# Optimization experiments

Hardware: AMD Instinct MI355X
Metric: run time of the kernel (lower is better)

Reference implementation:

```python
import jax, jax.numpy as jnp
from jax import lax
import numpy as np

B, C, HH, WW = 8, 64, 128, 128
N = HH * WW
EPS = 1e-5


def _roll_h(xn, sign):
    # per-channel cyclic roll along H: out[b,c,h,w] = xn[b,c,(h - sign*c) % H, w]
    _, Cx, Hx, _ = xn.shape
    c = jnp.arange(Cx)[:, None]
    idx = (jnp.arange(Hx)[None, :] - sign * jnp.arange(Cx)[:, None]) % Hx  # (C,H)
    return xn[:, c, idx, :]


def _roll_w(xn, sign):
    return _roll_h(xn.transpose(0, 1, 3, 2), sign).transpose(0, 1, 3, 2)


def _ch_linear(xn, w, b):
    # nn.Linear over the channel dim of a BCHW tensor (token-MLP on (B,N,C))
    return jnp.einsum('bchw,cd->bdhw', xn, w) + b[None, :, None, None]


def _bn(xn, g, b):
    # BatchNorm2d, training-mode stats (biased var over B,H,W)
    m = xn.mean(axis=(0, 2, 3), keepdims=True)
    v = xn.var(axis=(0, 2, 3), keepdims=True)
    return (xn - m) * lax.rsqrt(v + EPS) * g[None, :, None, None] + b[None, :, None, None]


def _dwconv(xn, w, dil, pad):
    return lax.conv_general_dilated(xn, w, (1, 1), ((pad, pad), (pad, pad)),
                                    rhs_dilation=(dil, dil),
                                    dimension_numbers=('NCHW', 'OIHW', 'NCHW'),
                                    feature_group_count=xn.shape[1])


def _pc(xn, w):
    # 1x1 pointwise conv, no bias; w: (C_out, C_in)
    return jnp.einsum('bchw,oc->bohw', xn, w)


def lgff_forward(x, fc1_w, fc1_b, fc2_w, fc2_b, fc3_w, fc3_b, fc4_w, fc4_b,
                 fc5_w, fc5_b, ln_g, ln_b, pc_w, dw_w, dw_b, dw_bn_g, dw_bn_b,
                 dd_w, dd_bn_g, dd_bn_b, se_w1, se_b1, se_w2, se_b2, H, W):
    Bx, Nx, Cx = x.shape
    xn = x.transpose(0, 2, 1).reshape(Bx, Cx, H, W)
    # branch 1: roll+c along H -> fc1 -> GELU -> roll+c along W -> fc2
    a = jax.nn.gelu(_ch_linear(_roll_h(xn, 1), fc1_w, fc1_b), approximate=False)
    x_1 = _ch_linear(_roll_w(a, 1), fc2_w, fc2_b) + xn
    # branch 2: roll-c along W -> fc3 -> GELU -> roll+c along H -> fc4
    b = jax.nn.gelu(_ch_linear(_roll_w(xn, -1), fc3_w, fc3_b), approximate=False)
    x_2 = _ch_linear(_roll_h(b, 1), fc4_w, fc4_b) + xn
    # concat along feature dim (token layout dim=2 == channel dim here), LayerNorm(2C), fc5
    xc = jnp.concatenate([x_1, x_2], axis=1)  # (B, 2C, H, W)
    m = xc.mean(axis=1, keepdims=True)
    v = xc.var(axis=1, keepdims=True)
    xc = (xc - m) * lax.rsqrt(v + EPS) * ln_g[None, :, None, None] + ln_b[None, :, None, None]
    x1 = _ch_linear(xc, fc5_w, fc5_b) + xn
    # conv fusion part
    x2 = _pc(x1, pc_w)
    y = jax.nn.relu(_bn(_dwconv(x2, dw_w, 1, 1) + dw_b[None, :, None, None], dw_bn_g, dw_bn_b))
    y = jax.nn.relu(_bn(_dwconv(y, dd_w, 2, 2), dd_bn_g, dd_bn_b))
    y = _pc(y, pc_w)
    # four branches x3..x6 share identical weights/input -> identical outputs
    x7 = 4.0 * (x2 * y)
    # SE block
    s = x7.mean(axis=(2, 3), keepdims=True)  # (B,C,1,1)
    e = jax.nn.relu(jnp.einsum('bcij,oc->boij', s, se_w1) + se_b1[None, :, None, None])
    e = jax.nn.sigmoid(jnp.einsum('bcij,oc->boij', e, se_w2) + se_b2[None, :, None, None])
    return x7 + x7 * e  # (B, C, H, W)


def setup_inputs():
    key = jax.random.key(0)
    ks = jax.random.split(key, 12)
    r = C // 8
    inp = {
        'x': jax.random.normal(ks[0], (B, N, C), jnp.float32),
        'fc1_w': jax.random.normal(ks[1], (C, C), jnp.float32) * 0.02,
        'fc1_b': jnp.zeros((C,), jnp.float32),
        'fc2_w': jax.random.normal(ks[2], (C, C), jnp.float32) * 0.02,
        'fc2_b': jnp.zeros((C,), jnp.float32),
        'fc3_w': jax.random.normal(ks[3], (C, C), jnp.float32) * 0.02,
        'fc3_b': jnp.zeros((C,), jnp.float32),
        'fc4_w': jax.random.normal(ks[4], (C, C), jnp.float32) * 0.02,
        'fc4_b': jnp.zeros((C,), jnp.float32),
        'fc5_w': jax.random.normal(ks[5], (2 * C, C), jnp.float32) * 0.02,
        'fc5_b': jnp.zeros((C,), jnp.float32),
        'ln_g': jnp.ones((2 * C,), jnp.float32),
        'ln_b': jnp.zeros((2 * C,), jnp.float32),
        'pc_w': jax.random.normal(ks[6], (C, C), jnp.float32) * np.sqrt(2.0 / C).astype(np.float32),
        'dw_w': jax.random.normal(ks[7], (C, 1, 3, 3), jnp.float32) * np.sqrt(2.0 / 9.0).astype(np.float32),
        'dw_b': jnp.zeros((C,), jnp.float32),
        'dw_bn_g': jnp.ones((C,), jnp.float32),
        'dw_bn_b': jnp.zeros((C,), jnp.float32),
        'dd_w': jax.random.normal(ks[8], (C, 1, 3, 3), jnp.float32) * np.sqrt(2.0 / 9.0).astype(np.float32),
        'dd_bn_g': jnp.ones((C,), jnp.float32),
        'dd_bn_b': jnp.zeros((C,), jnp.float32),
        'se_w1': jax.random.normal(ks[9], (r, C), jnp.float32) * np.sqrt(2.0 / r).astype(np.float32),
        'se_b1': jnp.zeros((r,), jnp.float32),
        'se_w2': jax.random.normal(ks[10], (C, r), jnp.float32) * np.sqrt(2.0 / C).astype(np.float32),
        'se_b2': jnp.zeros((C,), jnp.float32),
        'H': HH,
        'W': WW,
    }
    return inp


def reference(x, fc1_w, fc1_b, fc2_w, fc2_b, fc3_w, fc3_b, fc4_w, fc4_b,
              fc5_w, fc5_b, ln_g, ln_b, pc_w, dw_w, dw_b, dw_bn_g, dw_bn_b,
              dd_w, dd_bn_g, dd_bn_b, se_w1, se_b1, se_w2, se_b2, H, W):
    return lgff_forward(x, fc1_w, fc1_b, fc2_w, fc2_b, fc3_w, fc3_b, fc4_w, fc4_b,
                        fc5_w, fc5_b, ln_g, ln_b, pc_w, dw_w, dw_b, dw_bn_g, dw_bn_b,
                        dd_w, dd_bn_g, dd_bn_b, se_w1, se_b1, se_w2, se_b2, H, W)
```

## Files before the change

### kernel.cpp

```cpp
#include <hip/hip_runtime.h>

constexpr int NB  = 8;
constexpr int NC  = 64;
constexpr int NH  = 128;
constexpr int NW  = 128;
constexpr int NHW = NH * NW;
constexpr int CHW = NC * NHW;
constexpr int SZ  = NB * CHW;
constexpr int NPOS = NB * NHW;
constexpr float EPS = 1e-5f;

typedef unsigned short u16;
using bf8   = __attribute__((ext_vector_type(8))) short;
using u16x8 = __attribute__((ext_vector_type(8))) u16;
using u16x4 = __attribute__((ext_vector_type(4))) u16;
using f32x4 = __attribute__((ext_vector_type(4))) float;

static __device__ inline short f2bf(float f) {
    union { float f; unsigned int u; } v; v.f = f;
    unsigned int r = v.u + 0x7fffu + ((v.u >> 16) & 1u);
    return (short)(r >> 16);
}
static __device__ inline float bf2f(u16 u) {
    union { unsigned int i; float f; } v; v.i = ((unsigned int)u) << 16;
    return v.f;
}

__global__ void k_transpose(const float* __restrict__ x, u16* __restrict__ xn) {
    __shared__ float t[64 * 65];
    int b   = blockIdx.x >> 8;
    int hw0 = (blockIdx.x & 255) << 6;
    int tid = threadIdx.x;
    #pragma unroll
    for (int k = 0; k < 16; ++k) {
        int idx = tid + (k << 8);
        int c = idx & 63, hwl = idx >> 6;
        t[c * 65 + hwl] = x[((size_t)b * NHW + hw0 + hwl) * NC + c];
    }
    __syncthreads();
    #pragma unroll
    for (int k = 0; k < 16; ++k) {
        int idx = tid + (k << 8);
        int hwl = idx & 63, c = idx >> 6;
        xn[(size_t)(b * NC + c) * NHW + hw0 + hwl] = (u16)f2bf(t[c * 65 + hwl]);
    }
}

__global__ void k_pq(const float* __restrict__ w5, const float* __restrict__ lng,
                     const float* __restrict__ lnb, float* __restrict__ PQ) {
    int d = threadIdx.x;
    float P = 0.f, Q = 0.f;
    for (int c = 0; c < 128; ++c) {
        float wv = w5[c * 64 + d];
        P += lng[c] * wv;
        Q += lnb[c] * wv;
    }
    PQ[d] = P; PQ[64 + d] = Q;
}

__global__ __launch_bounds__(512) void
k_mfc2(const u16* __restrict__ xn,
       const float* __restrict__ w1, const float* __restrict__ b1,
       const float* __restrict__ w3, const float* __restrict__ b3,
       u16* __restrict__ t1, u16* __restrict__ t2) {
    __shared__ short wA[64 * 64];
    __shared__ short wB[64 * 64];
    int tid = threadIdx.x;
    int l = tid & 63, wv = tid >> 6;
    int q = l >> 4, col = l & 15;
    int bid = ((blockIdx.x & 7) << 7) | (blockIdx.x >> 3);

    {
        const float* wsrc = (wv < 4) ? w1 : w3;
        short* wdst = (wv < 4) ? wA : wB;
        int wv4 = wv & 3;
        #pragma unroll
        for (int i = 0; i < 8; ++i) {
            int c0 = wv4 * 2 + i * 8;
            unsigned int pk = (unsigned int)(u16)f2bf(wsrc[c0 * 64 + l]) |
                              ((unsigned int)(u16)f2bf(wsrc[(c0 + 1) * 64 + l]) << 16);
            *(unsigned int*)&wdst[l * 64 + (c0 ^ ((l & 7) << 3))] = pk;
        }
    }
    __syncthreads();

    int p  = bid * 128 + wv * 16 + col;
    int b  = p >> 14;
    int hw = p & (NHW - 1);
    int h  = hw >> 7, w = hw & 127;
    const u16* inb = xn + (size_t)b * CHW;

    f32x4 acc1[4], acc2[4];
    #pragma unroll
    for (int dt = 0; dt < 4; ++dt) {
        acc1[dt] = (f32x4){0.f, 0.f, 0.f, 0.f};
        acc2[dt] = (f32x4){0.f, 0.f, 0.f, 0.f};
    }
    #pragma unroll
    for (int ks = 0; ks < 2; ++ks) {
        bf8 f1, f2;
        #pragma unroll
        for (int j = 0; j < 8; ++j) {
            int c = ks * 32 + q * 8 + j;
            f1[j] = (short)inb[c * NHW + (((h - c) & 127) << 7) + w];
            f2[j] = (short)inb[c * NHW + (h << 7) + ((w + c) & 127)];
        }
        #pragma unroll
        for (int dt = 0; dt < 4; ++dt) {
            int d = dt * 16 + col;
            int wo = (ks * 32 + q * 8) ^ ((d & 7) << 3);
            acc1[dt] = __builtin_amdgcn_mfma_f32_16x16x32_bf16(f1, *(bf8*)&wA[d * 64 + wo], acc1[dt], 0, 0, 0);
            acc2[dt] = __builtin_amdgcn_mfma_f32_16x16x32_bf16(f2, *(bf8*)&wB[d * 64 + wo], acc2[dt], 0, 0, 0);
        }
    }

    int hwst = (bid * 128 + wv * 16 + q * 4) & (NHW - 1);
    size_t ob = (size_t)b * CHW + hwst;
    #pragma unroll
    for (int dt = 0; dt < 4; ++dt) {
        int d = dt * 16 + col;
        float bb1 = b1[d], bb3 = b3[d];
        u16x4 o1v, o2v;
        #pragma unroll
        for (int r = 0; r < 4; ++r) {
            float v1 = acc1[dt][r] + bb1;
            v1 = 0.5f * v1 * (1.f + erff(v1 * 0.70710678118654752f));
            float v2 = acc2[dt][r] + bb3;
            v2 = 0.5f * v2 * (1.f + erff(v2 * 0.70710678118654752f));
            o1v[r] = (u16)f2bf(v1);
            o2v[r] = (u16)f2bf(v2);
        }
        *(u16x4*)&t1[ob + (size_t)d * NHW] = o1v;
        *(u16x4*)&t2[ob + (size_t)d * NHW] = o2v;
    }
}

__global__ __launch_bounds__(512) void
k_ffuse(const u16* __restrict__ t1, const u16* __restrict__ t2,
        const u16* __restrict__ xnb,
        const float* __restrict__ fc2w, const float* __restrict__ fc2b,
        const float* __restrict__ fc4w, const float* __restrict__ fc4b,
        const float* __restrict__ w5, const float* __restrict__ lng,
        const float* __restrict__ PQ, const float* __restrict__ b5,
        u16* __restrict__ x1out) {
    __shared__ short wA[64 * 64];
    __shared__ short wB[64 * 64];
    __shared__ short wG[64 * 128];
    __shared__ short xt[128 * 140];

    int tid = threadIdx.x;
    int l = tid & 63, wv = tid >> 6;
    int q = l >> 4, col = l & 15;
    int bid = ((blockIdx.x & 7) << 7) | (blockIdx.x >> 3);

    {
        const float* wsrc = (wv < 4) ? fc2w : fc4w;
        short* wdst = (wv < 4) ? wA : wB;
        int wv4 = wv & 3;
        #pragma unroll
        for (int i = 0; i < 8; ++i) {
            int c0 = wv4 * 2 + i * 8;
            unsigned int pk = (unsigned int)(u16)f2bf(wsrc[c0 * 64 + l]) |
                              ((unsigned int)(u16)f2bf(wsrc[(c0 + 1) * 64 + l]) << 16);
            *(unsigned int*)&wdst[l * 64 + (c0 ^ ((l & 7) << 3))] = pk;
        }
    }
    #pragma unroll
    for (int i = 0; i < 8; ++i) {
        int c0 = wv * 2 + i * 16;
        unsigned int pk = (unsigned int)(u16)f2bf(lng[c0] * w5[c0 * 64 + l]) |
                          ((unsigned int)(u16)f2bf(lng[c0 + 1] * w5[(c0 + 1) * 64 + l]) << 16);
        *(unsigned int*)&wG[l * 128 + (c0 ^ ((l & 7) << 3))] = pk;
    }
    __syncthreads();

    int p  = bid * 128 + wv * 16 + col;
    int b  = p >> 14;
    int hw = p & (NHW - 1);
    int h  = hw >> 7, w = hw & 127;
    size_t base = (size_t)b * CHW;
    int pos = wv * 16 + col;

    f32x4 acc1[4], acc2[4];
    #pragma unroll
    for (int dt = 0; dt < 4; ++dt) {
        acc1[dt] = (f32x4){0.f, 0.f, 0.f, 0.f};
        acc2[dt] = (f32x4){0.f, 0.f, 0.f, 0.f};
    }
    #pragma unroll
    for (int ks = 0; ks < 2; ++ks) {
        bf8 f1, f2;
        #pragma unroll
        for (int j = 0; j < 8; ++j) {
            int c = ks * 32 + q * 8 + j;
            f1[j] = (short)t1[base + c * NHW + (h << 7) + ((w - c) & 127)];
            f2[j] = (short)t2[base + c * NHW + (((h - c) & 127) << 7) + w];
        }
        #pragma unroll
        for (int dt = 0; dt < 4; ++dt) {
            int d = dt * 16 + col;
            int wo = (ks * 32 + q * 8) ^ ((d & 7) << 3);
            acc1[dt] = __builtin_amdgcn_mfma_f32_16x16x32_bf16(*(bf8*)&wA[d * 64 + wo], f1, acc1[dt], 0, 0, 0);
            acc2[dt] = __builtin_amdgcn_mfma_f32_16x16x32_bf16(*(bf8*)&wB[d * 64 + wo], f2, acc2[dt], 0, 0, 0);
        }
    }

    float xr[16];
    #pragma unroll
    for (int dt = 0; dt < 4; ++dt)
        #pragma unroll
        for (int r = 0; r < 4; ++r)
            xr[dt * 4 + r] = bf2f(xnb[base + (size_t)(dt * 16 + q * 4 + r) * NHW + hw]);

    float s = 0.f, sq = 0.f;
    #pragma unroll
    for (int dt = 0; dt < 4; ++dt) {
        float v1[4], v2[4];
        #pragma unroll
        for (int r = 0; r < 4; ++r) {
            int d = dt * 16 + q * 4 + r;
            v1[r] = acc1[dt][r] + fc2b[d] + xr[dt * 4 + r];
            v2[r] = acc2[dt][r] + fc4b[d] + xr[dt * 4 + r];
            s += v1[r] + v2[r];
            sq += v1[r] * v1[r] + v2[r] * v2[r];
        }
        unsigned int pk0 = (unsigned int)(u16)f2bf(v1[0]) | ((unsigned int)(u16)f2bf(v1[1]) << 16);
        unsigned int pk1 = (unsigned int)(u16)f2bf(v1[2]) | ((unsigned int)(u16)f2bf(v1[3]) << 16);
        *(uint2*)&xt[pos * 140 + dt * 16 + q * 4] = make_uint2(pk0, pk1);
        unsigned int pk2 = (unsigned int)(u16)f2bf(v2[0]) | ((unsigned int)(u16)f2bf(v2[1]) << 16);
        unsigned int pk3 = (unsigned int)(u16)f2bf(v2[2]) | ((unsigned int)(u16)f2bf(v2[3]) << 16);
        *(uint2*)&xt[pos * 140 + 64 + dt * 16 + q * 4] = make_uint2(pk2, pk3);
    }
    s  += __shfl_xor(s, 16);  s += __shfl_xor(s, 32);
    sq += __shfl_xor(sq, 16); sq += __shfl_xor(sq, 32);
    float m    = s * (1.f / 128.f);
    float var  = sq * (1.f / 128.f) - m * m;
    float rstd = rsqrtf(var + EPS);
    float mr   = m * rstd;
    __syncthreads();

    f32x4 acc[4];
    #pragma unroll
    for (int dt = 0; dt < 4; ++dt) acc[dt] = (f32x4){0.f, 0.f, 0.f, 0.f};
    #pragma unroll
    for (int ks = 0; ks < 4; ++ks) {
        bf8 bfr = *(bf8*)&xt[pos * 140 + ks * 32 + q * 8];
        #pragma unroll
        for (int dt = 0; dt < 4; ++dt) {
            int d = dt * 16 + col;
            bf8 afr = *(bf8*)&wG[d * 128 + ((ks * 32 + q * 8) ^ ((d & 7) << 3))];
            acc[dt] = __builtin_amdgcn_mfma_f32_16x16x32_bf16(afr, bfr, acc[dt], 0, 0, 0);
        }
    }

    size_t obase = base + hw;
    #pragma unroll
    for (int dt = 0; dt < 4; ++dt) {
        #pragma unroll
        for (int r = 0; r < 4; ++r) {
            int d = dt * 16 + q * 4 + r;
            float val = rstd * acc[dt][r] + PQ[64 + d] - mr * PQ[d] + b5[d] + xr[dt * 4 + r];
            x1out[obase + (size_t)d * NHW] = (u16)f2bf(val);
        }
    }
}

template<bool BNRELU_IN, bool SEPART>
__global__ __launch_bounds__(512) void
k_mfc(const u16* __restrict__ in, const float* __restrict__ wgt,
      const float* __restrict__ psum, const float* __restrict__ psq,
      const float* __restrict__ bng, const float* __restrict__ bnb,
      const u16* __restrict__ x2in, float* __restrict__ gpart,
      u16* __restrict__ out) {
    __shared__ short wt[64 * 64];
    __shared__ float scl[64], sft[64];
    __shared__ float spart[8][64];
    int tid = threadIdx.x;
    int l = tid & 63, wv = tid >> 6;
    int q = l >> 4, col = l & 15;
    int bid = ((blockIdx.x & 7) << 7) | (blockIdx.x >> 3);

    #pragma unroll
    for (int i = 0; i < 8; ++i) {
        int d = wv * 8 + i;
        wt[d * 64 + (l ^ ((d & 7) << 3))] = f2bf(wgt[d * 64 + l]);
    }
    if (BNRELU_IN && tid < 64) {
        float s = 0.f, qv = 0.f;
        #pragma unroll
        for (int i = 0; i < 32; ++i) {
            int bb = i >> 2, j = i & 3;
            int idx = ((bb * 64 + tid) << 2) + j;
            s += psum[idx]; qv += psq[idx];
        }
        const float inv = 1.f / (float)(NB * NHW);
        float m = s * inv;
        float var = qv * inv - m * m;
        float rs = rsqrtf(var + EPS);
        float sc = rs * bng[tid];
        scl[tid] = sc;
        sft[tid] = bnb[tid] - m * sc;
    }
    __syncthreads();

    int p  = bid * 128 + wv * 16 + col;
    int b  = p >> 14;
    int hw = p & (NHW - 1);
    const u16* inb = in + (size_t)b * CHW;

    f32x4 acc[4];
    #pragma unroll
    for (int dt = 0; dt < 4; ++dt) acc[dt] = (f32x4){0.f, 0.f, 0.f, 0.f};

    #pragma unroll
    for (int ks = 0; ks < 2; ++ks) {
        bf8 bfr;
        #pragma unroll
        for (int j = 0; j < 8; ++j) {
            int c = ks * 32 + q * 8 + j;
            u16 raw = inb[c * NHW + hw];
            if (BNRELU_IN) {
                float v = fmaxf(bf2f(raw) * scl[c] + sft[c], 0.f);
                bfr[j] = f2bf(v);
            } else {
                bfr[j] = (short)raw;
            }
        }
        #pragma unroll
        for (int dt = 0; dt < 4; ++dt) {
            int d = dt * 16 + col;
            bf8 afr = *(bf8*)&wt[d * 64 + ((ks * 32 + q * 8) ^ ((d & 7) << 3))];
            acc[dt] = __builtin_amdgcn_mfma_f32_16x16x32_bf16(bfr, afr, acc[dt], 0, 0, 0);
        }
    }

    int hwst = (bid * 128 + wv * 16 + q * 4) & (NHW - 1);
    size_t ob = (size_t)b * CHW + hwst;
    float pp[4] = {0.f, 0.f, 0.f, 0.f};
    #pragma unroll
    for (int dt = 0; dt < 4; ++dt) {
        int d = dt * 16 + col;
        u16x4 ov;
        #pragma unroll
        for (int r = 0; r < 4; ++r) ov[r] = (u16)f2bf(acc[dt][r]);
        *(u16x4*)&out[ob + (size_t)d * NHW] = ov;
        if (SEPART) {
            u16x4 xv = *(const u16x4*)&x2in[ob + (size_t)d * NHW];
            #pragma unroll
            for (int r = 0; r < 4; ++r) pp[dt] += bf2f(xv[r]) * bf2f(ov[r]);
        }
    }

    if (SEPART) {
        #pragma unroll
        for (int dt = 0; dt < 4; ++dt) {
            pp[dt] += __shfl_xor(pp[dt], 16);
            pp[dt] += __shfl_xor(pp[dt], 32);
        }
        if (l < 16) {
            #pragma unroll
            for (int dt = 0; dt < 4; ++dt) spart[wv][dt * 16 + l] = pp[dt];
        }
        __syncthreads();
        if (tid < 64) {
            float s = 0.f;
            #pragma unroll
            for (int w8 = 0; w8 < 8; ++w8) s += spart[w8][tid];
            gpart[(size_t)bid * 64 + tid] = s;
        }
    }
}

__global__ void k_se_fin(const float* __restrict__ gpart, float* __restrict__ svec) {
    int b = blockIdx.x, c = threadIdx.x;
    float s = 0.f;
    for (int k = 0; k < 128; ++k) s += gpart[(size_t)(b * 128 + k) * 64 + c];
    svec[b * 64 + c] = s * (4.f / (float)NHW);
}

template<int DIL, bool HASBIAS, bool BNIN>
__global__ __launch_bounds__(256) void
k_dwlds(const u16* __restrict__ in, const float* __restrict__ wgt,
        const float* __restrict__ bias,
        const float* __restrict__ psumIn, const float* __restrict__ psqIn,
        const float* __restrict__ bng, const float* __restrict__ bnb,
        u16* __restrict__ out, float* __restrict__ psumOut, float* __restrict__ psqOut) {
    constexpr int STR = 136;
    __shared__ float tile[36 * STR];
    __shared__ float ss[256], sq[256];

    int blk = ((blockIdx.x & 7) << 8) | (blockIdx.x >> 3);
    int q   = blk & 3;
    int bc  = blk >> 2;
    int c   = bc & 63;
    int r0  = q * 32;
    int tid = threadIdx.x;
    const u16* ip = in + (size_t)bc * NHW;

    float scale = 0.f, shift = 0.f;
    if (BNIN) {
        float s = 0.f, qv = 0.f;
        #pragma unroll
        for (int i = 0; i < 32; ++i) {
            int bb = i >> 2, j = i & 3;
            int idx = ((bb * 64 + c) << 2) + j;
            s += psumIn[idx]; qv += psqIn[idx];
        }
        const float inv = 1.f / (float)(NB * NHW);
        float m = s * inv;
        float var = qv * inv - m * m;
        float rs = rsqrtf(var + EPS);
        scale = rs * bng[c];
        shift = bnb[c] - m * scale;
    }

    #pragma unroll 1
    for (int idx = tid; idx < 36 * 16; idx += 256) {
        int lr = idx >> 4, u = idx & 15;
        int gr = r0 - 2 + lr;
        float v[8] = {0.f, 0.f, 0.f, 0.f, 0.f, 0.f, 0.f, 0.f};
        if (gr >= 0 && gr < NH) {
            u16x8 raw = *(const u16x8*)(ip + gr * NW + u * 8);
            #pragma unroll
            for (int j = 0; j < 8; ++j) {
                float f = bf2f(raw[j]);
                if (BNIN) f = fmaxf(f * scale + shift, 0.f);
                v[j] = f;
            }
        }
        *(float4*)&tile[lr * STR + 4 + u * 8]     = make_float4(v[0], v[1], v[2], v[3]);
        *(float4*)&tile[lr * STR + 4 + u * 8 + 4] = make_float4(v[4], v[5], v[6], v[7]);
        if (u == 0)  *(float4*)&tile[lr * STR]       = make_float4(0.f, 0.f, 0.f, 0.f);
        if (u == 15) *(float4*)&tile[lr * STR + 132] = make_float4(0.f, 0.f, 0.f, 0.f);
    }
    __syncthreads();

    float wc[9];
    #pragma unroll
    for (int k = 0; k < 9; ++k) wc[k] = wgt[c * 9 + k];

    int row  = tid >> 3;
    int col0 = (tid & 7) * 16;
    float o[16];
    float bb = HASBIAS ? bias[c] : 0.f;
    #pragma unroll
    for (int j = 0; j < 16; ++j) o[j] = bb;

    #pragma unroll
    for (int i = 0; i < 3; ++i) {
        const float* rp = &tile[(row + 2 + (i - 1) * DIL) * STR + 4 + col0];
        float4 A  = *(const float4*)(rp - 4);
        float4 B0 = *(const float4*)(rp);
        float4 B1 = *(const float4*)(rp + 4);
        float4 B2 = *(const float4*)(rp + 8);
        float4 B3 = *(const float4*)(rp + 12);
        float4 Cc = *(const float4*)(rp + 16);
        float ww[24] = {A.x,A.y,A.z,A.w, B0.x,B0.y,B0.z,B0.w, B1.x,B1.y,B1.z,B1.w,
                        B2.x,B2.y,B2.z,B2.w, B3.x,B3.y,B3.z,B3.w, Cc.x,Cc.y,Cc.z,Cc.w};
        float w0 = wc[3 * i], w1 = wc[3 * i + 1], w2 = wc[3 * i + 2];
        #pragma unroll
        for (int j = 0; j < 16; ++j)
            o[j] += w0 * ww[4 + j - DIL] + w1 * ww[4 + j] + w2 * ww[4 + j + DIL];
    }

    u16* op = out + (size_t)bc * NHW + (r0 + row) * NW + col0;
    u16x8 o1, o2;
    #pragma unroll
    for (int j = 0; j < 8; ++j) { o1[j] = (u16)f2bf(o[j]); o2[j] = (u16)f2bf(o[8 + j]); }
    *(u16x8*)(op)     = o1;
    *(u16x8*)(op + 8) = o2;

    float s = 0.f, qq = 0.f;
    #pragma unroll
    for (int j = 0; j < 16; ++j) { s += o[j]; qq += o[j] * o[j]; }
    ss[tid] = s; sq[tid] = qq; __syncthreads();
    for (int off = 128; off > 0; off >>= 1) {
        if (tid < off) { ss[tid] += ss[tid + off]; sq[tid] += sq[tid + off]; }
        __syncthreads();
    }
    if (tid == 0) { psumOut[blk] = ss[0]; psqOut[blk] = sq[0]; }
}

__global__ void k_final8(const u16* __restrict__ x2, const u16* __restrict__ y3,
                         const float* __restrict__ svec,
                         const float* __restrict__ w1, const float* __restrict__ b1,
                         const float* __restrict__ w2, const float* __restrict__ b2,
                         float* __restrict__ out) {
    __shared__ float sh[64], e1[8], ev[1];
    int tid = threadIdx.x;
    int bc = blockIdx.x >> 3;
    int b  = bc >> 6, c = bc & 63;

    if (tid < 64) sh[tid] = svec[b * 64 + tid];
    __syncthreads();
    if (tid < 8) {
        float a = b1[tid];
        for (int cc = 0; cc < 64; ++cc) a += sh[cc] * w1[tid * 64 + cc];
        e1[tid] = a > 0.f ? a : 0.f;
    }
    __syncthreads();
    if (tid == 0) {
        float a = b2[c];
        #pragma unroll
        for (int j = 0; j < 8; ++j) a += e1[j] * w2[c * 8 + j];
        ev[0] = 1.f / (1.f + expf(-a));
    }
    __syncthreads();

    int t = blockIdx.x * 256 + tid;
    float f = 4.f * (1.f + ev[0]);
    u16x8 av = *(const u16x8*)(x2 + (size_t)t * 8);
    u16x8 bv = *(const u16x8*)(y3 + (size_t)t * 8);
    float4 o0, o1;
    o0.x = f * bf2f(av[0]) * bf2f(bv[0]); o0.y = f * bf2f(av[1]) * bf2f(bv[1]);
    o0.z = f * bf2f(av[2]) * bf2f(bv[2]); o0.w = f * bf2f(av[3]) * bf2f(bv[3]);
    o1.x = f * bf2f(av[4]) * bf2f(bv[4]); o1.y = f * bf2f(av[5]) * bf2f(bv[5]);
    o1.z = f * bf2f(av[6]) * bf2f(bv[6]); o1.w = f * bf2f(av[7]) * bf2f(bv[7]);
    *(float4*)(out + (size_t)t * 8)     = o0;
    *(float4*)(out + (size_t)t * 8 + 4) = o1;
}

extern "C" void kernel_launch(void* const* d_in, const int* in_sizes, int n_in,
                              void* d_out, int out_size, void* d_ws, size_t ws_size,
                              hipStream_t stream) {
    const float* x     = (const float*)d_in[0];
    const float* fc1w  = (const float*)d_in[1];
    const float* fc1b  = (const float*)d_in[2];
    const float* fc2w  = (const float*)d_in[3];
    const float* fc2b  = (const float*)d_in[4];
    const float* fc3w  = (const float*)d_in[5];
    const float* fc3b  = (const float*)d_in[6];
    const float* fc4w  = (const float*)d_in[7];
    const float* fc4b  = (const float*)d_in[8];
    const float* fc5w  = (const float*)d_in[9];
    const float* fc5b  = (const float*)d_in[10];
    const float* lng   = (const float*)d_in[11];
    const float* lnb   = (const float*)d_in[12];
    const float* pcw   = (const float*)d_in[13];
    const float* dww   = (const float*)d_in[14];
    const float* dwb   = (const float*)d_in[15];
    const float* dwbng = (const float*)d_in[16];
    const float* dwbnb = (const float*)d_in[17];
    const float* ddw   = (const float*)d_in[18];
    const float* ddbng = (const float*)d_in[19];
    const float* ddbnb = (const float*)d_in[20];
    const float* sew1  = (const float*)d_in[21];
    const float* seb1  = (const float*)d_in[22];
    const float* sew2  = (const float*)d_in[23];
    const float* seb2  = (const float*)d_in[24];

    float* out = (float*)d_out;
    u16* wsu = (u16*)d_ws;
    u16* bufA = wsu;
    u16* bufB = wsu + (size_t)SZ;
    u16* bufC = wsu + (size_t)2 * SZ;
    u16* bufD = wsu + (size_t)3 * SZ;
    float* st = (float*)(wsu + (size_t)4 * SZ);
    float* psumA = st;
    float* psqA  = st + 2048;
    float* psumB = st + 4096;
    float* psqB  = st + 6144;
    float* svec  = st + 8192;
    float* pqv   = st + 8704;
    float* gpart = st + 8832;

    dim3 blk(256);
    dim3 blk512(512);
    const float* nil = nullptr;
    const u16*   nilu = nullptr;
    float*       nilf = nullptr;

    k_transpose<<<NB * (NHW / 64), blk, 0, stream>>>(x, bufA);
    k_pq<<<1, 64, 0, stream>>>(fc5w, lng, lnb, pqv);
    k_mfc2<<<NPOS / 128, blk512, 0, stream>>>(bufA, fc1w, fc1b, fc3w, fc3b, bufB, bufC);
    k_ffuse<<<NPOS / 128, blk512, 0, stream>>>(bufB, bufC, bufA, fc2w, fc2b, fc4w, fc4b,
                                               fc5w, lng, pqv, fc5b, bufD);
    k_mfc<false, false><<<NPOS / 128, blk512, 0, stream>>>(bufD, pcw, nil, nil, nil, nil, nilu, nilf, bufA);
    k_dwlds<1, true, false><<<2048, blk, 0, stream>>>(bufA, dww, dwb, nil, nil, nil, nil, bufB, psumA, psqA);
    k_dwlds<2, false, true><<<2048, blk, 0, stream>>>(bufB, ddw, nil, psumA, psqA, dwbng, dwbnb, bufC, psumB, psqB);
    k_mfc<true, true><<<NPOS / 128, blk512, 0, stream>>>(bufC, pcw, psumB, psqB, ddbng, ddbnb, bufA, gpart, bufD);
    k_se_fin<<<NB, 64, 0, stream>>>(gpart, svec);
    k_final8<<<SZ / 2048, blk, 0, stream>>>(bufA, bufD, svec, sew1, seb1, sew2, seb2, out);
}
```

Baseline: 140.7 us.

## Fold PQ precompute into transpose launch and swap MFMA operands in ffuse

Removes the separate single-block k_pq launch by running it as an extra block of the transpose kernel, which saves one kernel launch. In k_ffuse, the MFMA operand order is swapped so each lane's accumulator holds 4 consecutive spatial positions for one output channel. This allows vectorized 4-wide residual loads and output stores along HW instead of scalar strided accesses. LayerNorm statistics now need a 16-lane shuffle reduction per row, and the LDS writes for the transposed tile become scalar, which may add bank conflicts.

```diff
diff --git a/kernel.cpp b/kernel.cpp
--- a/kernel.cpp
+++ b/kernel.cpp
@@ -26,7 +26,22 @@
     return v.f;
 }
 
-__global__ void k_transpose(const float* __restrict__ x, u16* __restrict__ xn) {
+__global__ void k_transpose(const float* __restrict__ x, u16* __restrict__ xn,
+                            const float* __restrict__ w5, const float* __restrict__ lng,
+                            const float* __restrict__ lnb, float* __restrict__ PQ) {
+    if (blockIdx.x == 2048) {
+        int d = threadIdx.x;
+        if (d < 64) {
+            float P = 0.f, Q = 0.f;
+            for (int c = 0; c < 128; ++c) {
+                float wv = w5[c * 64 + d];
+                P += lng[c] * wv;
+                Q += lnb[c] * wv;
+            }
+            PQ[d] = P; PQ[64 + d] = Q;
+        }
+        return;
+    }
     __shared__ float t[64 * 65];
     int b   = blockIdx.x >> 8;
     int hw0 = (blockIdx.x & 255) << 6;
@@ -44,18 +59,6 @@
         int hwl = idx & 63, c = idx >> 6;
         xn[(size_t)(b * NC + c) * NHW + hw0 + hwl] = (u16)f2bf(t[c * 65 + hwl]);
     }
-}
-
-__global__ void k_pq(const float* __restrict__ w5, const float* __restrict__ lng,
-                     const float* __restrict__ lnb, float* __restrict__ PQ) {
-    int d = threadIdx.x;
-    float P = 0.f, Q = 0.f;
-    for (int c = 0; c < 128; ++c) {
-        float wv = w5[c * 64 + d];
-        P += lng[c] * wv;
-        Q += lnb[c] * wv;
-    }
-    PQ[d] = P; PQ[64 + d] = Q;
 }
 
 __global__ __launch_bounds__(512) void
@@ -179,7 +182,6 @@
     int hw = p & (NHW - 1);
     int h  = hw >> 7, w = hw & 127;
     size_t base = (size_t)b * CHW;
-    int pos = wv * 16 + col;
 
     f32x4 acc1[4], acc2[4];
     #pragma unroll
@@ -200,43 +202,51 @@
         for (int dt = 0; dt < 4; ++dt) {
             int d = dt * 16 + col;
             int wo = (ks * 32 + q * 8) ^ ((d & 7) << 3);
-            acc1[dt] = __builtin_amdgcn_mfma_f32_16x16x32_bf16(*(bf8*)&wA[d * 64 + wo], f1, acc1[dt], 0, 0, 0);
-            acc2[dt] = __builtin_amdgcn_mfma_f32_16x16x32_bf16(*(bf8*)&wB[d * 64 + wo], f2, acc2[dt], 0, 0, 0);
-        }
-    }
-
-    float xr[16];
+            acc1[dt] = __builtin_amdgcn_mfma_f32_16x16x32_bf16(f1, *(bf8*)&wA[d * 64 + wo], acc1[dt], 0, 0, 0);
+            acc2[dt] = __builtin_amdgcn_mfma_f32_16x16x32_bf16(f2, *(bf8*)&wB[d * 64 + wo], acc2[dt], 0, 0, 0);
+        }
+    }
+
+    int hwst = (bid * 128 + wv * 16 + q * 4) & (NHW - 1);
+    size_t ob = base + hwst;
+    u16x4 xr4[4];
     #pragma unroll
     for (int dt = 0; dt < 4; ++dt)
-        #pragma unroll
-        for (int r = 0; r < 4; ++r)
-            xr[dt * 4 + r] = bf2f(xnb[base + (size_t)(dt * 16 + q * 4 + r) * NHW + hw]);
-
-    float s = 0.f, sq = 0.f;
+        xr4[dt] = *(const u16x4*)&xnb[ob + (size_t)(dt * 16 + col) * NHW];
+
+    float s[4] = {0.f, 0.f, 0.f, 0.f}, sq[4] = {0.f, 0.f, 0.f, 0.f};
+    int posr = wv * 16 + q * 4;
     #pragma unroll
     for (int dt = 0; dt < 4; ++dt) {
-        float v1[4], v2[4];
+        int d = dt * 16 + col;
+        float bb2 = fc2b[d], bb4 = fc4b[d];
         #pragma unroll
         for (int r = 0; r < 4; ++r) {
-            int d = dt * 16 + q * 4 + r;
-            v1[r] = acc1[dt][r] + fc2b[d] + xr[dt * 4 + r];
-            v2[r] = acc2[dt][r] + fc4b[d] + xr[dt * 4 + r];
-            s += v1[r] + v2[r];
-            sq += v1[r] * v1[r] + v2[r] * v2[r];
-        }
-        unsigned int pk0 = (unsigned int)(u16)f2bf(v1[0]) | ((unsigned int)(u16)f2bf(v1[1]) << 16);
-        unsigned int pk1 = (unsigned int)(u16)f2bf(v1[2]) | ((unsigned int)(u16)f2bf(v1[3]) << 16);
-        *(uint2*)&xt[pos * 140 + dt * 16 + q * 4] = make_uint2(pk0, pk1);
-        unsigned int pk2 = (unsigned int)(u16)f2bf(v2[0]) | ((unsigned int)(u16)f2bf(v2[1]) << 16);
-        unsigned int pk3 = (unsigned int)(u16)f2bf(v2[2]) | ((unsigned int)(u16)f2bf(v2[3]) << 16);
-        *(uint2*)&xt[pos * 140 + 64 + dt * 16 + q * 4] = make_uint2(pk2, pk3);
-    }
-    s  += __shfl_xor(s, 16);  s += __shfl_xor(s, 32);
-    sq += __shfl_xor(sq, 16); sq += __shfl_xor(sq, 32);
-    float m    = s * (1.f / 128.f);
-    float var  = sq * (1.f / 128.f) - m * m;
-    float rstd = rsqrtf(var + EPS);
-    float mr   = m * rstd;
+            float xv = bf2f(xr4[dt][r]);
+            float v1 = acc1[dt][r] + bb2 + xv;
+            float v2 = acc2[dt][r] + bb4 + xv;
+            s[r]  += v1 + v2;
+            sq[r] += v1 * v1 + v2 * v2;
+            xt[(posr + r) * 140 + d]      = f2bf(v1);
+            xt[(posr + r) * 140 + 64 + d] = f2bf(v2);
+        }
+    }
+    #pragma unroll
+    for (int off = 1; off < 16; off <<= 1) {
+        #pragma unroll
+        for (int r = 0; r < 4; ++r) {
+            s[r]  += __shfl_xor(s[r], off);
+            sq[r] += __shfl_xor(sq[r], off);
+        }
+    }
+    float rstd[4], mr[4];
+    #pragma unroll
+    for (int r = 0; r < 4; ++r) {
+        float m   = s[r] * (1.f / 128.f);
+        float var = sq[r] * (1.f / 128.f) - m * m;
+        rstd[r] = rsqrtf(var + EPS);
+        mr[r]   = m * rstd[r];
+    }
     __syncthreads();
 
     f32x4 acc[4];
@@ -244,24 +254,26 @@
     for (int dt = 0; dt < 4; ++dt) acc[dt] = (f32x4){0.f, 0.f, 0.f, 0.f};
     #pragma unroll
     for (int ks = 0; ks < 4; ++ks) {
-        bf8 bfr = *(bf8*)&xt[pos * 140 + ks * 32 + q * 8];
+        bf8 bfr = *(bf8*)&xt[(wv * 16 + col) * 140 + ks * 32 + q * 8];
         #pragma unroll
         for (int dt = 0; dt < 4; ++dt) {
             int d = dt * 16 + col;
-            bf8 afr = *(bf8*)&wG[d * 128 + ((ks * 32 + q * 8) ^ ((d & 7) << 3))];
-            acc[dt] = __builtin_amdgcn_mfma_f32_16x16x32_bf16(afr, bfr, acc[dt], 0, 0, 0);
-        }
-    }
-
-    size_t obase = base + hw;
+            bf8 wfr = *(bf8*)&wG[d * 128 + ((ks * 32 + q * 8) ^ ((d & 7) << 3))];
+            acc[dt] = __builtin_amdgcn_mfma_f32_16x16x32_bf16(bfr, wfr, acc[dt], 0, 0, 0);
+        }
+    }
+
     #pragma unroll
     for (int dt = 0; dt < 4; ++dt) {
+        int d = dt * 16 + col;
+        float pqd = PQ[d], pqq = PQ[64 + d], b5d = b5[d];
+        u16x4 ov;
         #pragma unroll
         for (int r = 0; r < 4; ++r) {
-            int d = dt * 16 + q * 4 + r;
-            float val = rstd * acc[dt][r] + PQ[64 + d] - mr * PQ[d] + b5[d] + xr[dt * 4 + r];
-            x1out[obase + (size_t)d * NHW] = (u16)f2bf(val);
-        }
+            float val = rstd[r] * acc[dt][r] + pqq - mr[r] * pqd + b5d + bf2f(xr4[dt][r]);
+            ov[r] = (u16)f2bf(val);
+        }
+        *(u16x4*)&x1out[ob + (size_t)d * NHW] = ov;
     }
 }
 
@@ -570,8 +582,7 @@
     const u16*   nilu = nullptr;
     float*       nilf = nullptr;
 
-    k_transpose<<<NB * (NHW / 64), blk, 0, stream>>>(x, bufA);
-    k_pq<<<1, 64, 0, stream>>>(fc5w, lng, lnb, pqv);
+    k_transpose<<<2049, blk, 0, stream>>>(x, bufA, fc5w, lng, lnb, pqv);
     k_mfc2<<<NPOS / 128, blk512, 0, stream>>>(bufA, fc1w, fc1b, fc3w, fc3b, bufB, bufC);
     k_ffuse<<<NPOS / 128, blk512, 0, stream>>>(bufB, bufC, bufA, fc2w, fc2b, fc4w, fc4b,
                                                fc5w, lng, pqv, fc5b, bufD);
```

After: 138.9 us. No clear change (-1.3%).
